# Optimization experiments

Hardware: AMD Instinct MI355X
Metric: run time of the kernel (lower is better)

Reference implementation:

```python
import jax, jax.numpy as jnp
import numpy as np
from jax import lax

B, S, H, X, C = 256, 512, 1024, 10, 10

def _kaiming(key, shape, fan_in):
    # torch kaiming_normal_ default: std = sqrt(2 / fan_in), created as (dim_out, dim_in) then .T
    return jax.random.normal(key, shape, dtype=jnp.float32) * np.float32(np.sqrt(2.0 / fan_in))

def setup_inputs() -> dict:
    key = jax.random.key(0)
    ks = jax.random.split(key, 12)
    inp = {
        "x": jax.random.randint(ks[0], (B, S), 0, X, dtype=jnp.int64),
        "Wx_g": _kaiming(ks[1], (X, H), X), "Wh_g": _kaiming(ks[2], (H, H), H), "b_g": jnp.zeros((H,), jnp.float32),
        "Wx_i": _kaiming(ks[3], (X, H), X), "Wh_i": _kaiming(ks[4], (H, H), H), "b_i": jnp.zeros((H,), jnp.float32),
        "Wx_f": _kaiming(ks[5], (X, H), X), "Wh_f": _kaiming(ks[6], (H, H), H), "b_f": jnp.zeros((H,), jnp.float32),
        "Wx_o": _kaiming(ks[7], (X, H), X), "Wh_o": _kaiming(ks[8], (H, H), H), "b_o": jnp.zeros((H,), jnp.float32),
        "Wp": _kaiming(ks[9], (H, C), H), "bp": jnp.zeros((C,), jnp.float32),
    }
    return inp

def reference(x, Wx_g, Wh_g, b_g, Wx_i, Wh_i, b_i, Wx_f, Wh_f, b_f, Wx_o, Wh_o, b_o, Wp, bp):
    # Stack the 4 gate projections into single [X,4H]/[H,4H] matmuls (same math,
    # gates recovered by slicing: order g|i|f|o).
    Wx = jnp.concatenate([Wx_g, Wx_i, Wx_f, Wx_o], axis=1)   # [X, 4H]
    Wh = jnp.concatenate([Wh_g, Wh_i, Wh_f, Wh_o], axis=1)   # [H, 4H]
    b = jnp.concatenate([b_g, b_i, b_f, b_o], axis=0)        # [4H]
    Hd = Wh_g.shape[0]
    xe = jax.nn.one_hot(x, Wx_g.shape[0], dtype=Wx.dtype)    # [B, S, X]
    xs = jnp.swapaxes(xe, 0, 1)                              # [S, B, X]

    h0 = jnp.zeros((x.shape[0], Hd), dtype=Wx.dtype)
    c0 = jnp.zeros((x.shape[0], Hd), dtype=Wx.dtype)

    def step(carry, xt):
        h, c = carry
        z = xt @ Wx + h @ Wh + b                             # [B, 4H]
        g = jnp.tanh(z[:, :Hd])
        i = jax.nn.sigmoid(z[:, Hd:2 * Hd])
        f = jax.nn.sigmoid(z[:, 2 * Hd:3 * Hd])
        o = jax.nn.sigmoid(z[:, 3 * Hd:])
        c = g * i + c * f
        h = jnp.tanh(c) * o
        return (h, c), None

    (h, _), _ = lax.scan(step, (h0, c0), xs)
    p = h @ Wp + bp                                          # logits from last timestep only
    return jax.nn.log_softmax(p, axis=1)
```

## Files before the change

kernel.cpp:

```cpp
#include <hip/hip_runtime.h>


typedef _Float16 half8 __attribute__((ext_vector_type(8)));
typedef float f32x4 __attribute__((ext_vector_type(4)));

#define HD 1024
#define SS 512
#define ZST 132

#define WS_FLAGS  0
#define WS_SLOT   2048
#define WS_FLAG   4096
#define WS_WXB    8192
#define WS_HBUF0  262144
#define WS_HBUF1  786432
#define WS_HFINAL 1310720

__device__ __forceinline__ float fast_sigmoid(float x) {
    return __builtin_amdgcn_rcpf(1.f + __expf(-x));
}
__device__ __forceinline__ float fast_tanh(float x) {
    float e = __expf(-2.f * x);
    return (1.f - e) * __builtin_amdgcn_rcpf(1.f + e);
}

__global__ void detect_kernel(const int* __restrict__ xw, int* __restrict__ flag) {
    int i = blockIdx.x * blockDim.x + threadIdx.x;
    if (xw[2 * i + 1] != 0) atomicOr(flag, 1);
}

__global__ void wxb_kernel(const float* __restrict__ Wxg, const float* __restrict__ bg,
                           const float* __restrict__ Wxi, const float* __restrict__ bi,
                           const float* __restrict__ Wxf, const float* __restrict__ bf,
                           const float* __restrict__ Wxo, const float* __restrict__ bo,
                           float* __restrict__ WxB) {
    int i = blockIdx.x * blockDim.x + threadIdx.x;
    if (i >= 4 * 10 * HD) return;
    int g = i / (10 * HD), r = i % (10 * HD), v = r / HD, j = r % HD;
    const float* Wx = (g == 0) ? Wxg : (g == 1) ? Wxi : (g == 2) ? Wxf : Wxo;
    const float* bb = (g == 0) ? bg  : (g == 1) ? bi  : (g == 2) ? bf  : bo;
    WxB[i] = Wx[v * HD + j] + bb[j];
}

__global__ void __launch_bounds__(256, 1)
lstm_main(const int* __restrict__ xraw, const float* __restrict__ Whg,
          const float* __restrict__ Whi, const float* __restrict__ Whf,
          const float* __restrict__ Who, unsigned char* __restrict__ ws)
{
    extern __shared__ char smem[];
    float* zbuf = (float*)smem;
    __shared__ int s_info;

    const int tid = threadIdx.x;
    const int w = tid >> 6, l = tid & 63;

    if (tid == 0) {
        unsigned int xcc;
        asm volatile("s_getreg_b32 %0, hwreg(HW_REG_XCC_ID)" : "=s"(xcc));
        unsigned int* slotc = (unsigned int*)(ws + WS_SLOT);
        unsigned int slot = __hip_atomic_fetch_add(&slotc[xcc & 7], 1u,
                                                   __ATOMIC_RELAXED, __HIP_MEMORY_SCOPE_AGENT);
        s_info = (int)(((xcc & 7) << 8) | (slot & 31));
    }
    __syncthreads();
    const int xcd  = (s_info >> 8) & 7;
    const int slot = s_info & 31;

    const int row0 = xcd << 5;
    const int col0 = slot << 5;
    const int u  = l & 15;
    const int kg = (l >> 4) << 3;
    const int kbase = w << 8;

    const int is32 = (*(const int*)(ws + WS_FLAG)) != 0;
    const float* WxB = (const float*)(ws + WS_WXB);
    _Float16* hb0 = (_Float16*)(ws + WS_HBUF0);
    _Float16* hb1 = (_Float16*)(ws + WS_HBUF1);
    float* hfinal = (float*)(ws + WS_HFINAL);
    unsigned int* flags = (unsigned int*)(ws + WS_FLAGS + xcd * 256);

    half8 bfrag[8][8];
#pragma unroll
    for (int nt = 0; nt < 8; ++nt) {
        const int g = nt >> 1;
        const float* Wmat = (g == 0) ? Whg : (g == 1) ? Whi : (g == 2) ? Whf : Who;
        const float* src = Wmat + (size_t)(kbase + kg) * HD + col0 + ((nt & 1) << 4) + u;
#pragma unroll
        for (int kk = 0; kk < 8; ++kk)
#pragma unroll
            for (int j = 0; j < 8; ++j)
                bfrag[kk][nt][j] = (_Float16)src[(size_t)(kk * 32 + j) * HD];
    }

    float cst[4] = {0.f, 0.f, 0.f, 0.f};

    for (int t = 0; t < SS; ++t) {
        const _Float16* hsrc = (t & 1) ? hb1 : hb0;
        _Float16*       hdst = (t & 1) ? hb0 : hb1;

        {
            const unsigned int tgt = (unsigned int)t;
            while (1) {
                unsigned int f = __hip_atomic_load(&flags[l & 31],
                                                   __ATOMIC_RELAXED, __HIP_MEMORY_SCOPE_AGENT);
                if (__all((int)(f >= tgt))) break;
                __builtin_amdgcn_s_sleep(1);
            }
        }

        const _Float16* aptr = hsrc + (size_t)(row0 + u) * HD + kbase + kg;
        half8 areg[8][2];
#pragma unroll
        for (int kk = 0; kk < 8; ++kk) {
#pragma unroll
            for (int mt = 0; mt < 2; ++mt)
                asm volatile("global_load_dwordx4 %0, %1, off sc0"
                             : "=v"(areg[kk][mt])
                             : "v"(aptr + (size_t)mt * 16 * HD + kk * 32));
        }

        f32x4 acc[2][8];
#pragma unroll
        for (int mt = 0; mt < 2; ++mt)
#pragma unroll
            for (int nt = 0; nt < 8; ++nt)
                acc[mt][nt] = (f32x4){0.f, 0.f, 0.f, 0.f};

#define DO_KK(KK, VM)                                                          \
        asm volatile("s_waitcnt vmcnt(" #VM ")" ::: "memory");                 \
        __builtin_amdgcn_sched_barrier(0);                                     \
        _Pragma("unroll")                                                      \
        for (int nt = 0; nt < 8; ++nt) {                                       \
            acc[0][nt] = __builtin_amdgcn_mfma_f32_16x16x32_f16(               \
                areg[KK][0], bfrag[KK][nt], acc[0][nt], 0, 0, 0);              \
            acc[1][nt] = __builtin_amdgcn_mfma_f32_16x16x32_f16(               \
                areg[KK][1], bfrag[KK][nt], acc[1][nt], 0, 0, 0);              \
        }
        DO_KK(0, 14) DO_KK(1, 12) DO_KK(2, 10) DO_KK(3, 8)
        DO_KK(4, 6)  DO_KK(5, 4)  DO_KK(6, 2)  DO_KK(7, 0)
#undef DO_KK

#pragma unroll
        for (int mt = 0; mt < 2; ++mt)
#pragma unroll
            for (int nt = 0; nt < 8; ++nt)
#pragma unroll
                for (int rr = 0; rr < 4; ++rr)
                    zbuf[(size_t)(w * 32 + mt * 16 + ((l >> 4) << 2) + rr) * ZST
                         + nt * 16 + u] = acc[mt][nt][rr];
        __syncthreads();

        const int lastt = (t == SS - 1);
#pragma unroll
        for (int q = 0; q < 4; ++q) {
            const int p = tid + (q << 8);
            const int m = p >> 5, uu = p & 31;
            const int brow = row0 + m;
            const size_t xi = (size_t)brow * SS + t;
            const int xv = is32 ? xraw[xi] : xraw[xi << 1];
            const int j = col0 + uu;
            float zg = WxB[(size_t)xv * HD + j];
            float zi = WxB[(size_t)(10 + xv) * HD + j];
            float zf = WxB[(size_t)(20 + xv) * HD + j];
            float zo = WxB[(size_t)(30 + xv) * HD + j];
#pragma unroll
            for (int wv = 0; wv < 4; ++wv) {
                const float* zr = zbuf + (size_t)(wv * 32 + m) * ZST;
                zg += zr[uu];
                zi += zr[32 + uu];
                zf += zr[64 + uu];
                zo += zr[96 + uu];
            }
            float gg = fast_tanh(zg);
            float ii = fast_sigmoid(zi);
            float ff = fast_sigmoid(zf);
            float oo = fast_sigmoid(zo);
            float cv = gg * ii + cst[q] * ff;
            cst[q] = cv;
            float hv = fast_tanh(cv) * oo;
            hdst[(size_t)brow * HD + j] = (_Float16)hv;
            if (lastt) hfinal[(size_t)brow * HD + j] = hv;
        }

        asm volatile("s_waitcnt vmcnt(0)" ::: "memory");
        __syncthreads();
        if (tid == 0)
            __hip_atomic_store(&flags[slot], (unsigned int)(t + 1),
                               __ATOMIC_RELAXED, __HIP_MEMORY_SCOPE_AGENT);
    }
}

__global__ void proj_kernel(const float* __restrict__ hfin, const float* __restrict__ Wp,
                            const float* __restrict__ bp, float* __restrict__ out)
{
    const int b = blockIdx.x;
    const int tid = threadIdx.x;
    float acc[10];
#pragma unroll
    for (int c = 0; c < 10; ++c) acc[c] = 0.f;
#pragma unroll
    for (int q = 0; q < 4; ++q) {
        int k = tid + (q << 8);
        float hv = hfin[b * HD + k];
#pragma unroll
        for (int c = 0; c < 10; ++c) acc[c] += hv * Wp[k * 10 + c];
    }
#pragma unroll
    for (int off = 32; off >= 1; off >>= 1)
#pragma unroll
        for (int c = 0; c < 10; ++c) acc[c] += __shfl_down(acc[c], off);

    __shared__ float red[4][10];
    const int wv = tid >> 6, ln = tid & 63;
    if (ln == 0)
#pragma unroll
        for (int c = 0; c < 10; ++c) red[wv][c] = acc[c];
    __syncthreads();
    if (tid == 0) {
        float p[10];
#pragma unroll
        for (int c = 0; c < 10; ++c)
            p[c] = red[0][c] + red[1][c] + red[2][c] + red[3][c] + bp[c];
        float mx = p[0];
#pragma unroll
        for (int c = 1; c < 10; ++c) mx = fmaxf(mx, p[c]);
        float s = 0.f;
#pragma unroll
        for (int c = 0; c < 10; ++c) s += __expf(p[c] - mx);
        float lse = mx + logf(s);
#pragma unroll
        for (int c = 0; c < 10; ++c) out[b * 10 + c] = p[c] - lse;
    }
}

extern "C" void kernel_launch(void* const* d_in, const int* in_sizes, int n_in,
                              void* d_out, int out_size, void* d_ws, size_t ws_size,
                              hipStream_t stream) {
    const int*   x   = (const int*)d_in[0];
    const float* Wxg = (const float*)d_in[1];
    const float* Whg = (const float*)d_in[2];
    const float* bg  = (const float*)d_in[3];
    const float* Wxi = (const float*)d_in[4];
    const float* Whi = (const float*)d_in[5];
    const float* bi  = (const float*)d_in[6];
    const float* Wxf = (const float*)d_in[7];
    const float* Whf = (const float*)d_in[8];
    const float* bf_ = (const float*)d_in[9];
    const float* Wxo = (const float*)d_in[10];
    const float* Who = (const float*)d_in[11];
    const float* bo  = (const float*)d_in[12];
    const float* Wp  = (const float*)d_in[13];
    const float* bp  = (const float*)d_in[14];
    unsigned char* ws = (unsigned char*)d_ws;
    float* out = (float*)d_out;

    hipMemsetAsync(ws, 0, 8192, stream);
    hipMemsetAsync(ws + WS_HBUF0, 0, 512 * 1024, stream);

    detect_kernel<<<16, 256, 0, stream>>>(x, (int*)(ws + WS_FLAG));
    wxb_kernel<<<160, 256, 0, stream>>>(Wxg, bg, Wxi, bi, Wxf, bf_, Wxo, bo,
                                        (float*)(ws + WS_WXB));

    const unsigned int smem_bytes = 98304;
    hipFuncSetAttribute((const void*)lstm_main,
                        hipFuncAttributeMaxDynamicSharedMemorySize, (int)smem_bytes);

    void* args[] = { (void*)&x, (void*)&Whg, (void*)&Whi, (void*)&Whf, (void*)&Who, (void*)&ws };
    hipError_t err = hipLaunchCooperativeKernel((const void*)lstm_main, dim3(256), dim3(256),
                                                args, smem_bytes, stream);
    if (err != hipSuccess) {
        lstm_main<<<dim3(256), dim3(256), smem_bytes, stream>>>(x, Whg, Whi, Whf, Who, ws);
    }

    proj_kernel<<<256, 256, 0, stream>>>((const float*)(ws + WS_HFINAL), Wp, bp, out);
}
```

Baseline: 3.342 ms.

## Prefetch input-projection terms before barrier wait and transpose LDS gate buffer

The per-step Wx+bias lookups and token reads are hoisted ahead of the inter-block flag spin, so their global-memory latency overlaps the wait. The spin is now done by one wave, without sleep, followed by a block barrier. The accumulator scratch in LDS is transposed so each MFMA result tile is written as one vector store, and the elementwise thread mapping is changed to match. This adds register pressure from the prefetched values and raises the risk of LDS bank conflicts on the strided reads.

```diff
diff --git a/kernel.cpp b/kernel.cpp
--- a/kernel.cpp
+++ b/kernel.cpp
@@ -6,7 +6,8 @@
 
 #define HD 1024
 #define SS 512
-#define ZST 132
+#define ROWP 36
+#define COLS 128
 
 #define WS_FLAGS  0
 #define WS_SLOT   2048
@@ -48,7 +49,7 @@
           const float* __restrict__ Who, unsigned char* __restrict__ ws)
 {
     extern __shared__ char smem[];
-    float* zbuf = (float*)smem;
+    float* zT = (float*)smem;
     __shared__ int s_info;
 
     const int tid = threadIdx.x;
@@ -92,21 +93,40 @@
                 bfrag[kk][nt][j] = (_Float16)src[(size_t)(kk * 32 + j) * HD];
     }
 
-    float cst[4] = {0.f, 0.f, 0.f, 0.f};
+    const int gm0 = tid >> 4;
+    const int gm1 = (tid + 256) >> 4;
+    const int gpr = tid & 15;
+    float cst[2][2] = {{0.f, 0.f}, {0.f, 0.f}};
 
     for (int t = 0; t < SS; ++t) {
         const _Float16* hsrc = (t & 1) ? hb1 : hb0;
         _Float16*       hdst = (t & 1) ? hb0 : hb1;
 
-        {
+        float wx[2][2][4];
+#pragma unroll
+        for (int q = 0; q < 2; ++q) {
+            const int m = q ? gm1 : gm0;
+            const size_t xi = (size_t)(row0 + m) * SS + t;
+            const int xv = is32 ? xraw[xi] : xraw[xi << 1];
+#pragma unroll
+            for (int ui = 0; ui < 2; ++ui) {
+                const int j = col0 + gpr + (ui << 4);
+#pragma unroll
+                for (int g = 0; g < 4; ++g)
+                    wx[q][ui][g] = WxB[(size_t)(g * 10 + xv) * HD + j];
+            }
+        }
+        __builtin_amdgcn_sched_barrier(0);
+
+        if (w == 0) {
             const unsigned int tgt = (unsigned int)t;
             while (1) {
                 unsigned int f = __hip_atomic_load(&flags[l & 31],
                                                    __ATOMIC_RELAXED, __HIP_MEMORY_SCOPE_AGENT);
                 if (__all((int)(f >= tgt))) break;
-                __builtin_amdgcn_s_sleep(1);
-            }
-        }
+            }
+        }
+        __syncthreads();
 
         const _Float16* aptr = hsrc + (size_t)(row0 + u) * HD + kbase + kg;
         half8 areg[8][2];
@@ -143,43 +163,42 @@
 #pragma unroll
         for (int mt = 0; mt < 2; ++mt)
 #pragma unroll
-            for (int nt = 0; nt < 8; ++nt)
-#pragma unroll
-                for (int rr = 0; rr < 4; ++rr)
-                    zbuf[(size_t)(w * 32 + mt * 16 + ((l >> 4) << 2) + rr) * ZST
-                         + nt * 16 + u] = acc[mt][nt][rr];
+            for (int nt = 0; nt < 8; ++nt) {
+                const int col = nt * 16 + u;
+                const int rowb = mt * 16 + ((l >> 4) << 2);
+                *(f32x4*)&zT[(size_t)w * COLS * ROWP + col * ROWP + rowb] = acc[mt][nt];
+            }
         __syncthreads();
 
         const int lastt = (t == SS - 1);
 #pragma unroll
-        for (int q = 0; q < 4; ++q) {
-            const int p = tid + (q << 8);
-            const int m = p >> 5, uu = p & 31;
+        for (int q = 0; q < 2; ++q) {
+            const int m = q ? gm1 : gm0;
             const int brow = row0 + m;
-            const size_t xi = (size_t)brow * SS + t;
-            const int xv = is32 ? xraw[xi] : xraw[xi << 1];
-            const int j = col0 + uu;
-            float zg = WxB[(size_t)xv * HD + j];
-            float zi = WxB[(size_t)(10 + xv) * HD + j];
-            float zf = WxB[(size_t)(20 + xv) * HD + j];
-            float zo = WxB[(size_t)(30 + xv) * HD + j];
-#pragma unroll
-            for (int wv = 0; wv < 4; ++wv) {
-                const float* zr = zbuf + (size_t)(wv * 32 + m) * ZST;
-                zg += zr[uu];
-                zi += zr[32 + uu];
-                zf += zr[64 + uu];
-                zo += zr[96 + uu];
-            }
-            float gg = fast_tanh(zg);
-            float ii = fast_sigmoid(zi);
-            float ff = fast_sigmoid(zf);
-            float oo = fast_sigmoid(zo);
-            float cv = gg * ii + cst[q] * ff;
-            cst[q] = cv;
-            float hv = fast_tanh(cv) * oo;
-            hdst[(size_t)brow * HD + j] = (_Float16)hv;
-            if (lastt) hfinal[(size_t)brow * HD + j] = hv;
+#pragma unroll
+            for (int ui = 0; ui < 2; ++ui) {
+                const int uu = gpr + (ui << 4);
+                const int j = col0 + uu;
+                float zv[4];
+#pragma unroll
+                for (int g = 0; g < 4; ++g) {
+                    float s = wx[q][ui][g];
+                    const int cb = (g * 32 + uu) * ROWP + m;
+#pragma unroll
+                    for (int wv = 0; wv < 4; ++wv)
+                        s += zT[wv * COLS * ROWP + cb];
+                    zv[g] = s;
+                }
+                float gg = fast_tanh(zv[0]);
+                float ii = fast_sigmoid(zv[1]);
+                float ff = fast_sigmoid(zv[2]);
+                float oo = fast_sigmoid(zv[3]);
+                float cv = gg * ii + cst[q][ui] * ff;
+                cst[q][ui] = cv;
+                float hv = fast_tanh(cv) * oo;
+                hdst[(size_t)brow * HD + j] = (_Float16)hv;
+                if (lastt) hfinal[(size_t)brow * HD + j] = hv;
+            }
         }
 
         asm volatile("s_waitcnt vmcnt(0)" ::: "memory");
```

New measurement: 2.984 ms. 10.7% less time.

## Split step flag wait into two halves and prefetch input projections early

Applied to the files above, without the earlier changes.

The per-step wait on all 32 producer flags is replaced by two narrower waits. Each wave waits on the 4 flags covering the first half of its K slice, issues those h loads, then waits on the flags for the second half. The one-hot input-projection loads (WxB gathers) now happen before the wait, so their latency overlaps the synchronisation instead of sitting on the gate-compute path. The s_sleep backoff is removed, which adds polling traffic, and the change relies on the flag-to-K-range mapping being correct.

```diff
diff --git a/kernel.cpp b/kernel.cpp
--- a/kernel.cpp
+++ b/kernel.cpp
@@ -94,30 +94,57 @@
 
     float cst[4] = {0.f, 0.f, 0.f, 0.f};
 
+    const unsigned int* myflag0 = &flags[(w << 3) + (l & 3)];
+    const unsigned int* myflag1 = &flags[(w << 3) + 4 + (l & 3)];
+
     for (int t = 0; t < SS; ++t) {
         const _Float16* hsrc = (t & 1) ? hb1 : hb0;
         _Float16*       hdst = (t & 1) ? hb0 : hb1;
-
-        {
-            const unsigned int tgt = (unsigned int)t;
-            while (1) {
-                unsigned int f = __hip_atomic_load(&flags[l & 31],
-                                                   __ATOMIC_RELAXED, __HIP_MEMORY_SCOPE_AGENT);
-                if (__all((int)(f >= tgt))) break;
-                __builtin_amdgcn_s_sleep(1);
-            }
-        }
+        const unsigned int tgt = (unsigned int)t;
+
+        float wx[4][4];
+#pragma unroll
+        for (int q = 0; q < 4; ++q) {
+            const int p = tid + (q << 8);
+            const int m = p >> 5, uu = p & 31;
+            const size_t xi = (size_t)(row0 + m) * SS + t;
+            const int xv = is32 ? xraw[xi] : xraw[xi << 1];
+            const int j = col0 + uu;
+#pragma unroll
+            for (int g = 0; g < 4; ++g)
+                wx[q][g] = WxB[(size_t)(g * 10 + xv) * HD + j];
+        }
+        __builtin_amdgcn_sched_barrier(0);
 
         const _Float16* aptr = hsrc + (size_t)(row0 + u) * HD + kbase + kg;
         half8 areg[8][2];
-#pragma unroll
-        for (int kk = 0; kk < 8; ++kk) {
+
+        while (1) {
+            unsigned int f = __hip_atomic_load(myflag0, __ATOMIC_RELAXED,
+                                               __HIP_MEMORY_SCOPE_AGENT);
+            if (__all((int)(f >= tgt))) break;
+        }
+        __builtin_amdgcn_sched_barrier(0);
+#pragma unroll
+        for (int kk = 0; kk < 4; ++kk)
 #pragma unroll
             for (int mt = 0; mt < 2; ++mt)
                 asm volatile("global_load_dwordx4 %0, %1, off sc0"
                              : "=v"(areg[kk][mt])
                              : "v"(aptr + (size_t)mt * 16 * HD + kk * 32));
-        }
+        while (1) {
+            unsigned int f = __hip_atomic_load(myflag1, __ATOMIC_RELAXED,
+                                               __HIP_MEMORY_SCOPE_AGENT);
+            if (__all((int)(f >= tgt))) break;
+        }
+        __builtin_amdgcn_sched_barrier(0);
+#pragma unroll
+        for (int kk = 4; kk < 8; ++kk)
+#pragma unroll
+            for (int mt = 0; mt < 2; ++mt)
+                asm volatile("global_load_dwordx4 %0, %1, off sc0"
+                             : "=v"(areg[kk][mt])
+                             : "v"(aptr + (size_t)mt * 16 * HD + kk * 32));
 
         f32x4 acc[2][8];
 #pragma unroll
@@ -136,8 +163,8 @@
             acc[1][nt] = __builtin_amdgcn_mfma_f32_16x16x32_f16(               \
                 areg[KK][1], bfrag[KK][nt], acc[1][nt], 0, 0, 0);              \
         }
-        DO_KK(0, 14) DO_KK(1, 12) DO_KK(2, 10) DO_KK(3, 8)
-        DO_KK(4, 6)  DO_KK(5, 4)  DO_KK(6, 2)  DO_KK(7, 0)
+        DO_KK(0, 8) DO_KK(1, 8) DO_KK(2, 8) DO_KK(3, 8)
+        DO_KK(4, 6) DO_KK(5, 4) DO_KK(6, 2) DO_KK(7, 0)
 #undef DO_KK
 
 #pragma unroll
@@ -156,13 +183,8 @@
             const int p = tid + (q << 8);
             const int m = p >> 5, uu = p & 31;
             const int brow = row0 + m;
-            const size_t xi = (size_t)brow * SS + t;
-            const int xv = is32 ? xraw[xi] : xraw[xi << 1];
             const int j = col0 + uu;
-            float zg = WxB[(size_t)xv * HD + j];
-            float zi = WxB[(size_t)(10 + xv) * HD + j];
-            float zf = WxB[(size_t)(20 + xv) * HD + j];
-            float zo = WxB[(size_t)(30 + xv) * HD + j];
+            float zg = wx[q][0], zi = wx[q][1], zf = wx[q][2], zo = wx[q][3];
 #pragma unroll
             for (int wv = 0; wv < 4; ++wv) {
                 const float* zr = zbuf + (size_t)(wv * 32 + m) * ZST;
```

Result: faster. 2.750 ms (-17.7%).
